# Performance work log

Hardware: AMD Instinct MI355X
Metric: run time of the kernel (lower is better)

## Reference

```python
import jax, jax.numpy as jnp
import numpy as np


def setup_inputs() -> dict:
    key = jax.random.key(0)
    ks = jax.random.split(key, 6)
    B, Tq, Tk = 4, 512, 512
    Q, K, C = 1024, 1024, 256
    query = jax.random.normal(ks[0], (B, Tq, Q), dtype=jnp.float32)
    kmat = jax.random.normal(ks[1], (B, Tk, K), dtype=jnp.float32)
    # Linear weights (torch nn.Linear stores [out, in]; we keep [in, out] for einsum)
    Wq = jax.random.normal(ks[2], (Q, C), dtype=jnp.float32) / np.sqrt(Q)
    Wk = jax.random.normal(ks[3], (K, C), dtype=jnp.float32) / np.sqrt(K)
    w_attn = jax.random.normal(ks[4], (C,), dtype=jnp.float32) / np.sqrt(C)
    b_attn = jax.random.normal(ks[5], (), dtype=jnp.float32) * 0.01
    return {"query": query, "key": kmat, "Wq": Wq, "Wk": Wk,
            "w_attn": w_attn, "b_attn": b_attn}


def reference(query, key, Wq, Wk, w_attn, b_attn):
    # Additive (Bahdanau) attention scores.
    # q2ctx: (B, Tq, C); k2ctx: (B, Tk, C)
    q2ctx = jnp.einsum('bqi,ic->bqc', query, Wq)
    k2ctx = jnp.einsum('bki,ic->bkc', key, Wk)
    # broadcast add -> (B, Tq, Tk, C), tanh, project to scalar and squeeze
    ctx = jnp.tanh(q2ctx[:, :, None, :] + k2ctx[:, None, :, :])
    scores = jnp.einsum('bqkc,c->bqk', ctx, w_attn) + b_attn
    return scores  # (B, Tq, Tk)
```

## Files before the change

### kernel.cpp

```cpp
#include <hip/hip_runtime.h>
#include <hip/hip_bf16.h>

#define M_ROWS 2048
#define KDIM   1024
#define CDIM   256
#define TQ     512
#define TK     512

#define GBM 64
#define GBN 32
#define GBK 32
#define NIT (KDIM / GBK)
#define DEPTH 4

#define SCALE2LOG2E 2.8853900817779268f

typedef __attribute__((ext_vector_type(8))) short short8;
typedef __attribute__((ext_vector_type(8))) unsigned short ushort8;
typedef __attribute__((ext_vector_type(4))) float floatx4;
typedef __attribute__((ext_vector_type(2))) float f32x2;

__device__ __forceinline__ short2 cvt2(float x, float y) {
    __hip_bfloat162 h = __float22bfloat162_rn(make_float2(x, y));
    short2 r;
    __builtin_memcpy(&r, &h, sizeof(r));
    return r;
}
__device__ __forceinline__ unsigned short f2bf1(float x) {
    return (unsigned short)cvt2(x, x).x;
}
__device__ __forceinline__ float bf2f(unsigned short u) {
    return __builtin_bit_cast(float, (unsigned)u << 16);
}
__device__ __forceinline__ f32x2 splat2(float x) { return (f32x2){x, x}; }

__global__ __launch_bounds__(256) void gemm_mfma_kernel(
    const float* __restrict__ Aq, const float* __restrict__ Ak,
    const float* __restrict__ Wq, const float* __restrict__ Wk,
    const float* __restrict__ w_attn,
    unsigned short* __restrict__ Eq, unsigned short* __restrict__ Ek)
{
    __shared__ short Ws[2][GBN][GBK + 8];

    const int z = blockIdx.z;
    const float* A = z ? Ak : Aq;
    const float* W = z ? Wk : Wq;
    unsigned short* E = z ? Ek : Eq;

    const int t    = threadIdx.x;
    const int lane = t & 63;
    const int wave = t >> 6;
    const int m0   = blockIdx.x * GBM;
    const int n0   = blockIdx.y * GBN;

    const int wr = t >> 3;
    const int wc = (t & 7) * 4;
    const int li = lane & 15;
    const int qd = lane >> 4;

    const int row = m0 + wave * 16 + li;
    const float* Arow = A + (size_t)row * KDIM + qd * 8;

    floatx4 acc0 = {0.f, 0.f, 0.f, 0.f};
    floatx4 acc1 = {0.f, 0.f, 0.f, 0.f};

    float4 pa0[DEPTH], pa1[DEPTH], pw[DEPTH];
    #pragma unroll
    for (int d = 0; d < DEPTH; ++d) {
        pa0[d] = *(const float4*)&Arow[d * GBK];
        pa1[d] = *(const float4*)&Arow[d * GBK + 4];
        pw[d]  = *(const float4*)&W[(size_t)(d * GBK + wr) * CDIM + n0 + wc];
    }

    {
        short2 u0 = cvt2(pw[0].x, pw[0].y), u1 = cvt2(pw[0].z, pw[0].w);
        Ws[0][wc + 0][wr] = u0.x;
        Ws[0][wc + 1][wr] = u0.y;
        Ws[0][wc + 2][wr] = u1.x;
        Ws[0][wc + 3][wr] = u1.y;
    }
    __syncthreads();

    #pragma unroll
    for (int it = 0; it < NIT; ++it) {
        const int buf = it & 1;
        const int s   = it & 3;
        short2 p0 = cvt2(pa0[s].x, pa0[s].y), p1 = cvt2(pa0[s].z, pa0[s].w);
        short2 p2 = cvt2(pa1[s].x, pa1[s].y), p3 = cvt2(pa1[s].z, pa1[s].w);
        short8 bv = { p0.x, p0.y, p1.x, p1.y, p2.x, p2.y, p3.x, p3.y };
        short8 af0 = *(const short8*)&Ws[buf][li][qd * 8];
        short8 af1 = *(const short8*)&Ws[buf][16 + li][qd * 8];
        acc0 = __builtin_amdgcn_mfma_f32_16x16x32_bf16(af0, bv, acc0, 0, 0, 0);
        acc1 = __builtin_amdgcn_mfma_f32_16x16x32_bf16(af1, bv, acc1, 0, 0, 0);
        if (it + 1 < NIT) {
            const int ns = (it + 1) & 3;
            short2 u0 = cvt2(pw[ns].x, pw[ns].y), u1 = cvt2(pw[ns].z, pw[ns].w);
            Ws[buf ^ 1][wc + 0][wr] = u0.x;
            Ws[buf ^ 1][wc + 1][wr] = u0.y;
            Ws[buf ^ 1][wc + 2][wr] = u1.x;
            Ws[buf ^ 1][wc + 3][wr] = u1.y;
        }
        if (it + DEPTH < NIT) {
            const int k0 = (it + DEPTH) * GBK;
            pa0[s] = *(const float4*)&Arow[k0];
            pa1[s] = *(const float4*)&Arow[k0 + 4];
            pw[s]  = *(const float4*)&W[(size_t)(k0 + wr) * CDIM + n0 + wc];
        }
        __syncthreads();
    }

    #pragma unroll
    for (int r = 0; r < 4; ++r) {
        const int c0 = n0 + qd * 4 + r;
        const int c1 = c0 + 16;
        float s0 = z ? 1.0f : (-0.5f / w_attn[c0]);
        float s1 = z ? 1.0f : (-0.5f / w_attn[c1]);
        float v0 = __builtin_amdgcn_exp2f(acc0[r] * SCALE2LOG2E) * s0;
        float v1 = __builtin_amdgcn_exp2f(acc1[r] * SCALE2LOG2E) * s1;
        E[(size_t)c0 * M_ROWS + row] = f2bf1(v0);
        E[(size_t)c1 * M_ROWS + row] = f2bf1(v1);
    }
}

__global__ __launch_bounds__(256) void bahdanau_kernel(
    const unsigned short* __restrict__ Eqs, const unsigned short* __restrict__ Ek,
    const float* __restrict__ w_attn, const float* __restrict__ b_attn,
    float* __restrict__ out)
{
    __shared__ union SMem {
        struct { float q[CDIM][36]; float k[CDIM][36]; } s;
        float red[16][4][64];
    } sm;
    __shared__ __align__(16) float sl[CDIM];
    __shared__ float partial[4];

    const int t    = threadIdx.x;
    const int b    = blockIdx.z;
    const int q0g  = blockIdx.x * 32;
    const int k0g  = blockIdx.y * 32;
    const int gq   = b * TQ + q0g;
    const int gk   = b * TK + k0g;
    const int wave = t >> 6;
    const int tl   = t & 63;
    const int q0   = (tl >> 3) * 4;
    const int k0   = (tl & 7) * 4;

    {
        float wv = w_attn[t];
        sl[t] = -0.5f / wv;
        float sum = wv;
        #pragma unroll
        for (int o = 32; o >= 1; o >>= 1) sum += __shfl_down(sum, o);
        if ((t & 63) == 0) partial[t >> 6] = sum;
    }

    const int sr = t >> 2;
    const int sc = (t & 3) * 8;
    ushort8 qv[4], kv[4];
    #pragma unroll
    for (int p = 0; p < 4; ++p) {
        qv[p] = *(const ushort8*)&Eqs[(size_t)(p * 64 + sr) * M_ROWS + gq + sc];
        kv[p] = *(const ushort8*)&Ek [(size_t)(p * 64 + sr) * M_ROWS + gk + sc];
    }
    #pragma unroll
    for (int p = 0; p < 4; ++p) {
        const int r = p * 64 + sr;
        *(float4*)&sm.s.q[r][sc]     = make_float4(bf2f(qv[p][0]), bf2f(qv[p][1]), bf2f(qv[p][2]), bf2f(qv[p][3]));
        *(float4*)&sm.s.q[r][sc + 4] = make_float4(bf2f(qv[p][4]), bf2f(qv[p][5]), bf2f(qv[p][6]), bf2f(qv[p][7]));
        *(float4*)&sm.s.k[r][sc]     = make_float4(bf2f(kv[p][0]), bf2f(kv[p][1]), bf2f(kv[p][2]), bf2f(kv[p][3]));
        *(float4*)&sm.s.k[r][sc + 4] = make_float4(bf2f(kv[p][4]), bf2f(kv[p][5]), bf2f(kv[p][6]), bf2f(kv[p][7]));
    }
    __syncthreads();

    f32x2 acc[4][2];
    #pragma unroll
    for (int qi = 0; qi < 4; ++qi) {
        acc[qi][0] = (f32x2){0.f, 0.f};
        acc[qi][1] = (f32x2){0.f, 0.f};
    }
    const int cb = wave * 64;
    #pragma unroll 2
    for (int cc = 0; cc < 64; cc += 4) {
        float4 s4 = *(const float4*)&sl[cb + cc];
        f32x2 qa[4][2], ka[4][2];
        #pragma unroll
        for (int j = 0; j < 4; ++j) {
            qa[j][0] = *(const f32x2*)&sm.s.q[cb + cc + j][q0];
            qa[j][1] = *(const f32x2*)&sm.s.q[cb + cc + j][q0 + 2];
            ka[j][0] = *(const f32x2*)&sm.s.k[cb + cc + j][k0];
            ka[j][1] = *(const f32x2*)&sm.s.k[cb + cc + j][k0 + 2];
        }
        #pragma unroll
        for (int qi = 0; qi < 4; ++qi) {
            const float qw0 = qa[0][qi >> 1][qi & 1];
            const float qw1 = qa[1][qi >> 1][qi & 1];
            const float qw2 = qa[2][qi >> 1][qi & 1];
            const float qw3 = qa[3][qi >> 1][qi & 1];
            #pragma unroll
            for (int kp = 0; kp < 2; ++kp) {
                f32x2 f1 = __builtin_elementwise_fma(splat2(qw0), ka[0][kp], splat2(s4.x));
                f32x2 f2 = __builtin_elementwise_fma(splat2(qw1), ka[1][kp], splat2(s4.y));
                f32x2 f3 = __builtin_elementwise_fma(splat2(qw2), ka[2][kp], splat2(s4.z));
                f32x2 f4 = __builtin_elementwise_fma(splat2(qw3), ka[3][kp], splat2(s4.w));
                f32x2 p12 = f1 * f2, p34 = f3 * f4;
                f32x2 s12 = f1 + f2, s34 = f3 + f4;
                f32x2 num = __builtin_elementwise_fma(s12, p34, s34 * p12);
                f32x2 den = p12 * p34;
                f32x2 r = {__builtin_amdgcn_rcpf(den.x), __builtin_amdgcn_rcpf(den.y)};
                acc[qi][kp] = __builtin_elementwise_fma(num, r, acc[qi][kp]);
            }
        }
    }

    __syncthreads();
    #pragma unroll
    for (int qi = 0; qi < 4; ++qi) {
        #pragma unroll
        for (int kp = 0; kp < 2; ++kp) {
            sm.red[qi * 4 + kp * 2 + 0][wave][tl] = acc[qi][kp].x;
            sm.red[qi * 4 + kp * 2 + 1][wave][tl] = acc[qi][kp].y;
        }
    }
    __syncthreads();

    const float bias2 = *b_attn + partial[0] + partial[1] + partial[2] + partial[3];
    const int L  = t & 63;
    const int i  = t >> 6;
    const int qr = (L >> 3) * 4 + i;
    const int kc = (L & 7) * 4;
    float4 v;
    #pragma unroll
    for (int j = 0; j < 4; ++j) {
        float s = sm.red[i * 4 + j][0][L] + sm.red[i * 4 + j][1][L]
                + sm.red[i * 4 + j][2][L] + sm.red[i * 4 + j][3][L];
        (&v.x)[j] = s + bias2;
    }
    *(float4*)&out[((size_t)b * TQ + q0g + qr) * TK + k0g + kc] = v;
}

extern "C" void kernel_launch(void* const* d_in, const int* in_sizes, int n_in,
                              void* d_out, int out_size, void* d_ws, size_t ws_size,
                              hipStream_t stream) {
    const float* query  = (const float*)d_in[0];
    const float* key    = (const float*)d_in[1];
    const float* Wq     = (const float*)d_in[2];
    const float* Wk     = (const float*)d_in[3];
    const float* w_attn = (const float*)d_in[4];
    const float* b_attn = (const float*)d_in[5];
    float* out = (float*)d_out;

    unsigned short* Eqs = (unsigned short*)d_ws;
    unsigned short* Ek  = Eqs + (size_t)CDIM * M_ROWS;

    dim3 gemm_grid(M_ROWS / GBM, CDIM / GBN, 2);
    gemm_mfma_kernel<<<gemm_grid, 256, 0, stream>>>(query, key, Wq, Wk, w_attn, Eqs, Ek);

    dim3 main_grid(TQ / 32, TK / 32, 4);
    bahdanau_kernel<<<main_grid, 256, 0, stream>>>(Eqs, Ek, w_attn, b_attn, out);
}
```

Measured before the change: 112.1 us.

## Shrink GEMM prefetch depth and split Bahdanau C-dim staging into two phases

The GEMM kernel drops from a four-deep register prefetch with a double-buffered LDS tile to a two-deep prefetch with a single LDS buffer and two barriers per iteration. The Bahdanau kernel stages the C dimension in two halves of 128, halving its LDS footprint, prefetching the second half while computing the first, and declares launch bounds of 4 blocks per CU. The aim is lower register and LDS pressure so more blocks fit per CU. The cost is an extra barrier per GEMM iteration and an extra sync phase in the attention kernel.

```diff
diff --git a/kernel.cpp b/kernel.cpp
--- a/kernel.cpp
+++ b/kernel.cpp
@@ -10,8 +10,6 @@
 #define GBM 64
 #define GBN 32
 #define GBK 32
-#define NIT (KDIM / GBK)
-#define DEPTH 4
 
 #define SCALE2LOG2E 2.8853900817779268f
 
@@ -40,7 +38,7 @@
     const float* __restrict__ w_attn,
     unsigned short* __restrict__ Eq, unsigned short* __restrict__ Ek)
 {
-    __shared__ short Ws[2][GBN][GBK + 8];
+    __shared__ short Ws[GBN][GBK + 8];
 
     const int z = blockIdx.z;
     const float* A = z ? Ak : Aq;
@@ -64,49 +62,36 @@
     floatx4 acc0 = {0.f, 0.f, 0.f, 0.f};
     floatx4 acc1 = {0.f, 0.f, 0.f, 0.f};
 
-    float4 pa0[DEPTH], pa1[DEPTH], pw[DEPTH];
-    #pragma unroll
-    for (int d = 0; d < DEPTH; ++d) {
-        pa0[d] = *(const float4*)&Arow[d * GBK];
-        pa1[d] = *(const float4*)&Arow[d * GBK + 4];
-        pw[d]  = *(const float4*)&W[(size_t)(d * GBK + wr) * CDIM + n0 + wc];
-    }
-
-    {
-        short2 u0 = cvt2(pw[0].x, pw[0].y), u1 = cvt2(pw[0].z, pw[0].w);
-        Ws[0][wc + 0][wr] = u0.x;
-        Ws[0][wc + 1][wr] = u0.y;
-        Ws[0][wc + 2][wr] = u1.x;
-        Ws[0][wc + 3][wr] = u1.y;
-    }
-    __syncthreads();
-
-    #pragma unroll
-    for (int it = 0; it < NIT; ++it) {
-        const int buf = it & 1;
-        const int s   = it & 3;
+    float4 pa0[2], pa1[2], pw[2];
+    pa0[0] = *(const float4*)&Arow[0];
+    pa1[0] = *(const float4*)&Arow[4];
+    pw[0]  = *(const float4*)&W[(size_t)wr * CDIM + n0 + wc];
+    pa0[1] = *(const float4*)&Arow[GBK];
+    pa1[1] = *(const float4*)&Arow[GBK + 4];
+    pw[1]  = *(const float4*)&W[(size_t)(GBK + wr) * CDIM + n0 + wc];
+
+    for (int it = 0; it < KDIM / GBK; ++it) {
+        const int s = it & 1;
+        __syncthreads();
+        short2 u0 = cvt2(pw[s].x, pw[s].y), u1 = cvt2(pw[s].z, pw[s].w);
+        Ws[wc + 0][wr] = u0.x;
+        Ws[wc + 1][wr] = u0.y;
+        Ws[wc + 2][wr] = u1.x;
+        Ws[wc + 3][wr] = u1.y;
         short2 p0 = cvt2(pa0[s].x, pa0[s].y), p1 = cvt2(pa0[s].z, pa0[s].w);
         short2 p2 = cvt2(pa1[s].x, pa1[s].y), p3 = cvt2(pa1[s].z, pa1[s].w);
         short8 bv = { p0.x, p0.y, p1.x, p1.y, p2.x, p2.y, p3.x, p3.y };
-        short8 af0 = *(const short8*)&Ws[buf][li][qd * 8];
-        short8 af1 = *(const short8*)&Ws[buf][16 + li][qd * 8];
-        acc0 = __builtin_amdgcn_mfma_f32_16x16x32_bf16(af0, bv, acc0, 0, 0, 0);
-        acc1 = __builtin_amdgcn_mfma_f32_16x16x32_bf16(af1, bv, acc1, 0, 0, 0);
-        if (it + 1 < NIT) {
-            const int ns = (it + 1) & 3;
-            short2 u0 = cvt2(pw[ns].x, pw[ns].y), u1 = cvt2(pw[ns].z, pw[ns].w);
-            Ws[buf ^ 1][wc + 0][wr] = u0.x;
-            Ws[buf ^ 1][wc + 1][wr] = u0.y;
-            Ws[buf ^ 1][wc + 2][wr] = u1.x;
-            Ws[buf ^ 1][wc + 3][wr] = u1.y;
-        }
-        if (it + DEPTH < NIT) {
-            const int k0 = (it + DEPTH) * GBK;
+        __syncthreads();
+        if (it + 2 < KDIM / GBK) {
+            const int k0 = (it + 2) * GBK;
             pa0[s] = *(const float4*)&Arow[k0];
             pa1[s] = *(const float4*)&Arow[k0 + 4];
             pw[s]  = *(const float4*)&W[(size_t)(k0 + wr) * CDIM + n0 + wc];
         }
-        __syncthreads();
+        short8 af0 = *(const short8*)&Ws[li][qd * 8];
+        short8 af1 = *(const short8*)&Ws[16 + li][qd * 8];
+        acc0 = __builtin_amdgcn_mfma_f32_16x16x32_bf16(af0, bv, acc0, 0, 0, 0);
+        acc1 = __builtin_amdgcn_mfma_f32_16x16x32_bf16(af1, bv, acc1, 0, 0, 0);
     }
 
     #pragma unroll
@@ -122,13 +107,13 @@
     }
 }
 
-__global__ __launch_bounds__(256) void bahdanau_kernel(
+__global__ __launch_bounds__(256, 4) void bahdanau_kernel(
     const unsigned short* __restrict__ Eqs, const unsigned short* __restrict__ Ek,
     const float* __restrict__ w_attn, const float* __restrict__ b_attn,
     float* __restrict__ out)
 {
     __shared__ union SMem {
-        struct { float q[CDIM][36]; float k[CDIM][36]; } s;
+        struct { float q[128][36]; float k[128][36]; } s;
         float red[16][4][64];
     } sm;
     __shared__ __align__(16) float sl[CDIM];
@@ -154,23 +139,14 @@
         if ((t & 63) == 0) partial[t >> 6] = sum;
     }
 
-    const int sr = t >> 2;
-    const int sc = (t & 3) * 8;
-    ushort8 qv[4], kv[4];
-    #pragma unroll
-    for (int p = 0; p < 4; ++p) {
-        qv[p] = *(const ushort8*)&Eqs[(size_t)(p * 64 + sr) * M_ROWS + gq + sc];
-        kv[p] = *(const ushort8*)&Ek [(size_t)(p * 64 + sr) * M_ROWS + gk + sc];
-    }
-    #pragma unroll
-    for (int p = 0; p < 4; ++p) {
-        const int r = p * 64 + sr;
-        *(float4*)&sm.s.q[r][sc]     = make_float4(bf2f(qv[p][0]), bf2f(qv[p][1]), bf2f(qv[p][2]), bf2f(qv[p][3]));
-        *(float4*)&sm.s.q[r][sc + 4] = make_float4(bf2f(qv[p][4]), bf2f(qv[p][5]), bf2f(qv[p][6]), bf2f(qv[p][7]));
-        *(float4*)&sm.s.k[r][sc]     = make_float4(bf2f(kv[p][0]), bf2f(kv[p][1]), bf2f(kv[p][2]), bf2f(kv[p][3]));
-        *(float4*)&sm.s.k[r][sc + 4] = make_float4(bf2f(kv[p][4]), bf2f(kv[p][5]), bf2f(kv[p][6]), bf2f(kv[p][7]));
-    }
-    __syncthreads();
+    const int sr = t >> 1;
+    const int sc = (t & 1) * 16;
+
+    ushort8 qv[2], kv[2];
+    qv[0] = *(const ushort8*)&Eqs[(size_t)sr * M_ROWS + gq + sc];
+    qv[1] = *(const ushort8*)&Eqs[(size_t)sr * M_ROWS + gq + sc + 8];
+    kv[0] = *(const ushort8*)&Ek [(size_t)sr * M_ROWS + gk + sc];
+    kv[1] = *(const ushort8*)&Ek [(size_t)sr * M_ROWS + gk + sc + 8];
 
     f32x2 acc[4][2];
     #pragma unroll
@@ -178,41 +154,62 @@
         acc[qi][0] = (f32x2){0.f, 0.f};
         acc[qi][1] = (f32x2){0.f, 0.f};
     }
-    const int cb = wave * 64;
-    #pragma unroll 2
-    for (int cc = 0; cc < 64; cc += 4) {
-        float4 s4 = *(const float4*)&sl[cb + cc];
-        f32x2 qa[4][2], ka[4][2];
-        #pragma unroll
-        for (int j = 0; j < 4; ++j) {
-            qa[j][0] = *(const f32x2*)&sm.s.q[cb + cc + j][q0];
-            qa[j][1] = *(const f32x2*)&sm.s.q[cb + cc + j][q0 + 2];
-            ka[j][0] = *(const f32x2*)&sm.s.k[cb + cc + j][k0];
-            ka[j][1] = *(const f32x2*)&sm.s.k[cb + cc + j][k0 + 2];
-        }
-        #pragma unroll
-        for (int qi = 0; qi < 4; ++qi) {
-            const float qw0 = qa[0][qi >> 1][qi & 1];
-            const float qw1 = qa[1][qi >> 1][qi & 1];
-            const float qw2 = qa[2][qi >> 1][qi & 1];
-            const float qw3 = qa[3][qi >> 1][qi & 1];
+
+    #pragma unroll
+    for (int ph = 0; ph < 2; ++ph) {
+        *(float4*)&sm.s.q[sr][sc]      = make_float4(bf2f(qv[0][0]), bf2f(qv[0][1]), bf2f(qv[0][2]), bf2f(qv[0][3]));
+        *(float4*)&sm.s.q[sr][sc + 4]  = make_float4(bf2f(qv[0][4]), bf2f(qv[0][5]), bf2f(qv[0][6]), bf2f(qv[0][7]));
+        *(float4*)&sm.s.q[sr][sc + 8]  = make_float4(bf2f(qv[1][0]), bf2f(qv[1][1]), bf2f(qv[1][2]), bf2f(qv[1][3]));
+        *(float4*)&sm.s.q[sr][sc + 12] = make_float4(bf2f(qv[1][4]), bf2f(qv[1][5]), bf2f(qv[1][6]), bf2f(qv[1][7]));
+        *(float4*)&sm.s.k[sr][sc]      = make_float4(bf2f(kv[0][0]), bf2f(kv[0][1]), bf2f(kv[0][2]), bf2f(kv[0][3]));
+        *(float4*)&sm.s.k[sr][sc + 4]  = make_float4(bf2f(kv[0][4]), bf2f(kv[0][5]), bf2f(kv[0][6]), bf2f(kv[0][7]));
+        *(float4*)&sm.s.k[sr][sc + 8]  = make_float4(bf2f(kv[1][0]), bf2f(kv[1][1]), bf2f(kv[1][2]), bf2f(kv[1][3]));
+        *(float4*)&sm.s.k[sr][sc + 12] = make_float4(bf2f(kv[1][4]), bf2f(kv[1][5]), bf2f(kv[1][6]), bf2f(kv[1][7]));
+        __syncthreads();
+
+        if (ph == 0) {
+            qv[0] = *(const ushort8*)&Eqs[(size_t)(128 + sr) * M_ROWS + gq + sc];
+            qv[1] = *(const ushort8*)&Eqs[(size_t)(128 + sr) * M_ROWS + gq + sc + 8];
+            kv[0] = *(const ushort8*)&Ek [(size_t)(128 + sr) * M_ROWS + gk + sc];
+            kv[1] = *(const ushort8*)&Ek [(size_t)(128 + sr) * M_ROWS + gk + sc + 8];
+        }
+
+        const int cb = wave * 32;
+        #pragma unroll 2
+        for (int cc = 0; cc < 32; cc += 4) {
+            float4 s4 = *(const float4*)&sl[ph * 128 + cb + cc];
+            f32x2 qa[4][2], ka[4][2];
             #pragma unroll
-            for (int kp = 0; kp < 2; ++kp) {
-                f32x2 f1 = __builtin_elementwise_fma(splat2(qw0), ka[0][kp], splat2(s4.x));
-                f32x2 f2 = __builtin_elementwise_fma(splat2(qw1), ka[1][kp], splat2(s4.y));
-                f32x2 f3 = __builtin_elementwise_fma(splat2(qw2), ka[2][kp], splat2(s4.z));
-                f32x2 f4 = __builtin_elementwise_fma(splat2(qw3), ka[3][kp], splat2(s4.w));
-                f32x2 p12 = f1 * f2, p34 = f3 * f4;
-                f32x2 s12 = f1 + f2, s34 = f3 + f4;
-                f32x2 num = __builtin_elementwise_fma(s12, p34, s34 * p12);
-                f32x2 den = p12 * p34;
-                f32x2 r = {__builtin_amdgcn_rcpf(den.x), __builtin_amdgcn_rcpf(den.y)};
-                acc[qi][kp] = __builtin_elementwise_fma(num, r, acc[qi][kp]);
+            for (int j = 0; j < 4; ++j) {
+                qa[j][0] = *(const f32x2*)&sm.s.q[cb + cc + j][q0];
+                qa[j][1] = *(const f32x2*)&sm.s.q[cb + cc + j][q0 + 2];
+                ka[j][0] = *(const f32x2*)&sm.s.k[cb + cc + j][k0];
+                ka[j][1] = *(const f32x2*)&sm.s.k[cb + cc + j][k0 + 2];
             }
-        }
-    }
-
-    __syncthreads();
+            #pragma unroll
+            for (int qi = 0; qi < 4; ++qi) {
+                const float qw0 = qa[0][qi >> 1][qi & 1];
+                const float qw1 = qa[1][qi >> 1][qi & 1];
+                const float qw2 = qa[2][qi >> 1][qi & 1];
+                const float qw3 = qa[3][qi >> 1][qi & 1];
+                #pragma unroll
+                for (int kp = 0; kp < 2; ++kp) {
+                    f32x2 f1 = __builtin_elementwise_fma(splat2(qw0), ka[0][kp], splat2(s4.x));
+                    f32x2 f2 = __builtin_elementwise_fma(splat2(qw1), ka[1][kp], splat2(s4.y));
+                    f32x2 f3 = __builtin_elementwise_fma(splat2(qw2), ka[2][kp], splat2(s4.z));
+                    f32x2 f4 = __builtin_elementwise_fma(splat2(qw3), ka[3][kp], splat2(s4.w));
+                    f32x2 p12 = f1 * f2, p34 = f3 * f4;
+                    f32x2 s12 = f1 + f2, s34 = f3 + f4;
+                    f32x2 num = __builtin_elementwise_fma(s12, p34, s34 * p12);
+                    f32x2 den = p12 * p34;
+                    f32x2 r = {__builtin_amdgcn_rcpf(den.x), __builtin_amdgcn_rcpf(den.y)};
+                    acc[qi][kp] = __builtin_elementwise_fma(num, r, acc[qi][kp]);
+                }
+            }
+        }
+        __syncthreads();
+    }
+
     #pragma unroll
     for (int qi = 0; qi < 4; ++qi) {
         #pragma unroll
```

After: 110.4 us. No clear change (-1.5%).
